# Kernel optimization log

Hardware: AMD Instinct MI355X
Metric: run time of the kernel (lower is better)

Reference implementation:

```python
import jax, jax.numpy as jnp
import numpy as np

L = 16384   # sequence length
H = 1024    # feature dim
P = 1024    # state dim (ssm_size=2048, conj_sym=True -> P = ssm_size//2)
STEP_RESCALE = 1.0
CLIP_MAX = -1e-4


def setup_inputs() -> dict:
    key = jax.random.key(0)
    ks = jax.random.split(key, 7)
    log_dt_min, log_dt_max = np.log(0.001), np.log(0.1)
    return {
        "input_sequence": jax.random.normal(ks[0], (L, H), jnp.float32),
        # stable eigenvalues: negative real part
        "Lambda_re": -(jnp.abs(jax.random.normal(ks[1], (P,), jnp.float32)) + 1e-3),
        "Lambda_im": jax.random.normal(ks[2], (P,), jnp.float32) * jnp.pi,
        "B": jax.random.normal(ks[3], (P, H, 2), jnp.float32) / np.sqrt(H),
        "C": jax.random.normal(ks[4], (H, P, 2), jnp.float32) / np.sqrt(P),
        "D": jax.random.normal(ks[5], (H,), jnp.float32),
        "log_step": jax.random.uniform(ks[6], (P, 1), jnp.float32,
                                        minval=log_dt_min, maxval=log_dt_max),
    }


def _binop(q_i, q_j):
    # binary operator of the linear recurrence (diagonal A)
    A_i, b_i = q_i
    A_j, b_j = q_j
    return (A_j * A_i, A_j * b_i + b_j)


def reference(input_sequence, Lambda_re, Lambda_im, B, C, D, log_step):
    # clip_eigs=True: clamp real part at -1e-4
    Lambda = jnp.minimum(Lambda_re, CLIP_MAX) + 1j * Lambda_im        # (P,) complex64
    B_tilde = B[..., 0] + 1j * B[..., 1]                              # (P, H)
    C_tilde = C[..., 0] + 1j * C[..., 1]                              # (H, P)
    step = STEP_RESCALE * jnp.exp(log_step[:, 0])                     # (P,)
    # ZOH discretisation
    Lambda_bar = jnp.exp(Lambda * step)                               # (P,)
    B_bar = ((Lambda_bar - 1.0) / Lambda)[:, None] * B_tilde          # (P, H)
    # input projection: (L,H) @ (H,P) -> (L,P) complex
    Bu = input_sequence.astype(B_bar.dtype) @ B_bar.T
    Lam = jnp.broadcast_to(Lambda_bar, Bu.shape)                      # (L, P)
    # parallel (Blelchley-style) associative scan over time
    _, xs = jax.lax.associative_scan(_binop, (Lam, Bu))               # (L, P)
    # output projection; conj_sym=True -> factor 2 on the real part
    ys = 2.0 * jnp.real(xs @ C_tilde.T)                               # (L, H)
    return ys + input_sequence * D
```

## Files before the change

kernel.cpp:

```cpp
#include <hip/hip_runtime.h>
#include <hip/hip_bf16.h>
#include <stdint.h>


#define L_SEQ 16384
#define H_DIM 1024
#define P_DIM 1024
#define NCH   256
#define TCH   64

typedef __bf16 bf16x8 __attribute__((ext_vector_type(8)));
typedef float  floatx4 __attribute__((ext_vector_type(4)));
using bf16 = __hip_bfloat16;

__device__ __forceinline__ void gld_lds16(const void* g, void* l) {
    __builtin_amdgcn_global_load_lds(
        (const __attribute__((address_space(1))) uint32_t*)g,
        (__attribute__((address_space(3))) uint32_t*)l, 16, 0, 0);
}

__device__ __forceinline__ float lo_bf(uint32_t v) { return __uint_as_float(v << 16); }
__device__ __forceinline__ float hi_bf(uint32_t v) { return __uint_as_float(v & 0xffff0000u); }
__device__ __forceinline__ uint32_t pack_bf(float r, float i) {
    bf16 rb = __float2bfloat16(r), ib = __float2bfloat16(i);
    return ((uint32_t)(*(uint16_t*)&ib) << 16) | (uint32_t)(*(uint16_t*)&rb);
}

__device__ __forceinline__ float rd(const void* p, size_t i, int f) {
    return f ? ((const float*)p)[i]
             : __bfloat162float(((const bf16*)p)[i]);
}

__device__ __forceinline__ int detect_f32(const uint16_t* u) {
    __shared__ int cnt;
    if (threadIdx.x == 0) cnt = 0;
    __syncthreads();
    int c = 0;
    #pragma unroll
    for (int i = 0; i < 8; ++i) {
        int e = (u[threadIdx.x * 8 + i] >> 7) & 0xFF;
        c += (e >= 134);
    }
    if (c) atomicAdd(&cnt, c);
    __syncthreads();
    return cnt > 32;
}

__global__ void convert_u(const void* __restrict__ uin, bf16* __restrict__ ub) {
    const int f = detect_f32((const uint16_t*)uin);
    const size_t g = (size_t)blockIdx.x * 256 + threadIdx.x;
    if (f) {
        const float4* s = (const float4*)uin + g * 2;
        float4 a = s[0], b = s[1];
        alignas(16) bf16 t[8] = {
            __float2bfloat16(a.x), __float2bfloat16(a.y),
            __float2bfloat16(a.z), __float2bfloat16(a.w),
            __float2bfloat16(b.x), __float2bfloat16(b.y),
            __float2bfloat16(b.z), __float2bfloat16(b.w)};
        ((uint4*)ub)[g] = *(const uint4*)t;
    } else {
        ((uint4*)ub)[g] = ((const uint4*)uin)[g];
    }
}

__global__ void prep_all(const void* __restrict__ u,
                         const void* __restrict__ Lre, const void* __restrict__ Lim,
                         const void* __restrict__ lstep, const void* __restrict__ B,
                         const void* __restrict__ C, const void* __restrict__ D,
                         bf16* __restrict__ W1t, bf16* __restrict__ W2t,
                         float* __restrict__ d_f,
                         float2* __restrict__ lam, float2* __restrict__ lamT) {
    const int f = detect_f32((const uint16_t*)u);
    const int p = blockIdx.x;
    float lr = fminf(rd(Lre, p, f), -1e-4f);
    float li = rd(Lim, p, f);
    float s  = expf(rd(lstep, p, f));
    float ea = expf(lr * s);
    float lbr = ea * cosf(li * s), lbi = ea * sinf(li * s);
    float dr = lbr - 1.0f, di = lbi;
    float den = lr * lr + li * li;
    float cr = (dr * lr + di * li) / den;
    float ci = (di * lr - dr * li) / den;
    if (threadIdx.x == 0) {
        lam[p] = make_float2(lbr, lbi);
        float tr = lbr, ti = lbi;
        #pragma unroll
        for (int q = 0; q < 6; ++q) {
            float nr = tr * tr - ti * ti, ni = 2.0f * tr * ti;
            tr = nr; ti = ni;
        }
        lamT[p] = make_float2(tr, ti);
        d_f[p] = rd(D, p, f);
    }
    for (int h = threadIdx.x; h < H_DIM; h += blockDim.x) {
        size_t base = ((size_t)p * H_DIM + h) * 2;
        float br = rd(B, base + 0, f);
        float bi = rd(B, base + 1, f);
        W1t[(size_t)(2 * p)     * H_DIM + h] = __float2bfloat16(cr * br - ci * bi);
        W1t[(size_t)(2 * p + 1) * H_DIM + h] = __float2bfloat16(cr * bi + ci * br);
    }
    const int h = blockIdx.x;
    for (int q = threadIdx.x; q < P_DIM; q += blockDim.x) {
        size_t base = ((size_t)h * P_DIM + q) * 2;
        W2t[(size_t)h * (2 * P_DIM) + 2 * q]     = __float2bfloat16( 2.0f * rd(C, base + 0, f));
        W2t[(size_t)h * (2 * P_DIM) + 2 * q + 1] = __float2bfloat16(-2.0f * rd(C, base + 1, f));
    }
}

template <int N, int K, int MODE>
__global__ __launch_bounds__(256) void gemm_bt(
    const bf16* __restrict__ A, const bf16* __restrict__ Bt,
    bf16* __restrict__ OutBF, float* __restrict__ OutF,
    const bf16* __restrict__ U, const float* __restrict__ Dvec,
    const float2* __restrict__ lam, float2* __restrict__ aggp) {
    constexpr int NXB = N / 128;
    __shared__ alignas(16) uint8_t smem[32768];
    uint8_t* sA = smem;
    uint8_t* sB = smem + 16384;

    const int tid  = threadIdx.x;
    const int wave = tid >> 6;
    const int lane = tid & 63;
    const int bid = blockIdx.x;
    const int xr  = bid & 7;
    const int jj  = bid >> 3;
    const int bx  = jj % NXB;
    const int by  = (jj / NXB) * 8 + xr;
    const int bm  = by * 128, bn = bx * 128;
    const int wm  = (wave >> 1) * 64, wn = (wave & 1) * 64;

    floatx4 acc[4][4] = {};

    const int fr   = lane & 15;
    const int kq   = lane >> 4;
    const int srow = tid >> 3;
    const int skc  = tid & 7;

    for (int k0 = 0; k0 < K; k0 += 64) {
        #pragma unroll
        for (int q = 0; q < 4; ++q) {
            const int row = q * 32 + srow;
            const int kcg = skc ^ (row & 7);
            gld_lds16(A  + (size_t)(bm + row) * K + k0 + kcg * 8,
                      sA + q * 4096 + wave * 1024);
            gld_lds16(Bt + (size_t)(bn + row) * K + k0 + kcg * 8,
                      sB + q * 4096 + wave * 1024);
        }
        __syncthreads();
        #pragma unroll
        for (int s = 0; s < 2; ++s) {
            bf16x8 af[4], bfr[4];
            #pragma unroll
            for (int mi = 0; mi < 4; ++mi) {
                const int row = wm + mi * 16 + fr;
                const int ch  = (s * 4 + kq) ^ (row & 7);
                af[mi] = *(const bf16x8*)(sA + row * 128 + ch * 16);
            }
            #pragma unroll
            for (int ni = 0; ni < 4; ++ni) {
                const int row = wn + ni * 16 + fr;
                const int ch  = (s * 4 + kq) ^ (row & 7);
                bfr[ni] = *(const bf16x8*)(sB + row * 128 + ch * 16);
            }
            #pragma unroll
            for (int mi = 0; mi < 4; ++mi)
                #pragma unroll
                for (int ni = 0; ni < 4; ++ni)
                    acc[mi][ni] = __builtin_amdgcn_mfma_f32_16x16x32_bf16(
                        af[mi], bfr[ni], acc[mi][ni], 0, 0, 0);
        }
        __syncthreads();
    }

    const int col0  = bn + wn + fr;
    const int rbase = bm + wm + kq * 4;
    #pragma unroll
    for (int mi = 0; mi < 4; ++mi) {
        #pragma unroll
        for (int rr = 0; rr < 4; ++rr) {
            const int row = rbase + mi * 16 + rr;
            #pragma unroll
            for (int ni = 0; ni < 4; ++ni) {
                const int c = col0 + ni * 16;
                float v = acc[mi][ni][rr];
                if (MODE == 2) {
                    float uu = __bfloat162float(U[(size_t)row * H_DIM + c]);
                    __builtin_nontemporal_store(v + uu * Dvec[c],
                                                &OutF[(size_t)row * N + c]);
                } else {
                    OutBF[(size_t)row * N + c] = __float2bfloat16(v);
                }
            }
        }
    }

    if (MODE == 1) {
        float2* wtab = (float2*)smem;
        {
            const int ql = tid >> 2;
            const int t0 = (tid & 3) * 16;
            float2 lb = lam[(bn >> 1) + ql];
            float tr = lb.x, ti = lb.y;
            #pragma unroll
            for (int q = 0; q < 4; ++q) {
                float nr = tr * tr - ti * ti, ni = 2.f * tr * ti;
                tr = nr; ti = ni;
            }
            float p32r = tr * tr - ti * ti, p32i = 2.f * tr * ti;
            float wr, wi;
            if (t0 == 0)       { wr = p32r * tr - p32i * ti; wi = p32r * ti + p32i * tr; }
            else if (t0 == 16) { wr = p32r; wi = p32i; }
            else if (t0 == 32) { wr = tr;   wi = ti; }
            else               { wr = 1.f;  wi = 0.f; }
            #pragma unroll
            for (int j = 15; j >= 0; --j) {
                wtab[ql * 64 + t0 + j] = make_float2(wr, wi);
                float nr = wr * lb.x - wi * lb.y;
                float ni = wr * lb.y + wi * lb.x;
                wr = nr; wi = ni;
            }
        }
        __syncthreads();
        const int par = fr & 1;
        const int cg  = (bm + wm) >> 6;
        #pragma unroll
        for (int ni = 0; ni < 4; ++ni) {
            const int ql = (wn + ni * 16 + (fr & ~1)) >> 1;
            float s = 0.f;
            #pragma unroll
            for (int mi = 0; mi < 4; ++mi)
                #pragma unroll
                for (int rr = 0; rr < 4; ++rr) {
                    const int t = mi * 16 + kq * 4 + rr;
                    float own  = acc[mi][ni][rr];
                    float part = __shfl_xor(own, 1);
                    float2 wv = wtab[ql * 64 + t];
                    s += wv.x * own + (par ? wv.y : -wv.y) * part;
                }
            s += __shfl_xor(s, 16);
            s += __shfl_xor(s, 32);
            float other = __shfl_xor(s, 1);
            if (kq == 0 && par == 0)
                aggp[(size_t)cg * P_DIM + (bn >> 1) + ql] = make_float2(s, other);
        }
    }
}

__global__ void scan_phase2p(const float2* __restrict__ agg,
                             const float2* __restrict__ lamT,
                             float2* __restrict__ carry) {
    const int w = threadIdx.x >> 6;
    const int j = threadIdx.x & 63;
    const int p = blockIdx.x * 4 + w;
    const float2 A = lamT[p];
    float b2r = A.x * A.x - A.y * A.y, b2i = 2.f * A.x * A.y;
    float Br = b2r * b2r - b2i * b2i, Bi = 2.f * b2r * b2i;
    float2 a[4];
    #pragma unroll
    for (int k = 0; k < 4; ++k) a[k] = agg[(size_t)(4 * j + k) * P_DIM + p];
    float xr = 0.f, xi = 0.f;
    #pragma unroll
    for (int k = 0; k < 4; ++k) {
        float nr = A.x * xr - A.y * xi + a[k].x;
        float ni = A.x * xi + A.y * xr + a[k].y;
        xr = nr; xi = ni;
    }
    float cr = Br, ci = Bi, vr = xr, vi = xi;
    #pragma unroll
    for (int d = 1; d < 64; d <<= 1) {
        float pvr = __shfl_up(vr, d), pvi = __shfl_up(vi, d);
        float pcr = __shfl_up(cr, d), pci = __shfl_up(ci, d);
        if (j >= d) {
            float nvr = cr * pvr - ci * pvi + vr;
            float nvi = cr * pvi + ci * pvr + vi;
            float ncr = cr * pcr - ci * pci;
            float nci = cr * pci + ci * pcr;
            vr = nvr; vi = nvi; cr = ncr; ci = nci;
        }
    }
    float sr = __shfl_up(vr, 1), si = __shfl_up(vi, 1);
    if (j == 0) { sr = 0.f; si = 0.f; }
    #pragma unroll
    for (int k = 0; k < 4; ++k) {
        carry[(size_t)(4 * j + k) * P_DIM + p] = make_float2(sr, si);
        float nr = A.x * sr - A.y * si + a[k].x;
        float ni = A.x * si + A.y * sr + a[k].y;
        sr = nr; si = ni;
    }
}

__global__ void scan_phase3(uint32_t* __restrict__ BuX,
                            const float2* __restrict__ lam,
                            const float2* __restrict__ carry) {
    const int p = blockIdx.y * 256 + threadIdx.x;
    const int c = blockIdx.x;
    const float2 lb = lam[p];
    const float2 c0 = carry[(size_t)c * P_DIM + p];
    float xr = c0.x, xi = c0.y;
    uint32_t* b = BuX + (size_t)c * TCH * P_DIM + p;
    #pragma unroll 4
    for (int j = 0; j < TCH; ++j) {
        uint32_t v = *b;
        float nr = lb.x * xr - lb.y * xi + lo_bf(v);
        float ni = lb.x * xi + lb.y * xr + hi_bf(v);
        xr = nr; xi = ni;
        *b = pack_bf(xr, xi);
        b += P_DIM;
    }
}

extern "C" void kernel_launch(void* const* d_in, const int* in_sizes, int n_in,
                              void* d_out, int out_size, void* d_ws, size_t ws_size,
                              hipStream_t stream) {
    float* out = (float*)d_out;

    char* w = (char*)d_ws;
    w += 256;
    float2* lam   = (float2*)w;  w += (size_t)P_DIM * 8;
    float2* lamT  = (float2*)w;  w += (size_t)P_DIM * 8;
    float*  d_f   = (float*)w;   w += (size_t)H_DIM * 4;
    float2* agg   = (float2*)w;  w += (size_t)NCH * P_DIM * 8;
    float2* carry = (float2*)w;  w += (size_t)NCH * P_DIM * 8;
    bf16*   W1t   = (bf16*)w;    w += (size_t)2 * P_DIM * H_DIM * 2;
    bf16*   W2t   = (bf16*)w;    w += (size_t)H_DIM * 2 * P_DIM * 2;
    bf16*   ub    = (bf16*)w;    w += (size_t)L_SEQ * H_DIM * 2;
    bf16*   Xbuf  = (bf16*)w;

    convert_u<<<(L_SEQ * H_DIM / 8) / 256, 256, 0, stream>>>(d_in[0], ub);
    prep_all<<<P_DIM, 256, 0, stream>>>(d_in[0], d_in[1], d_in[2], d_in[6],
                                        d_in[3], d_in[4], d_in[5],
                                        W1t, W2t, d_f, lam, lamT);

    gemm_bt<2 * P_DIM, H_DIM, 1><<<(2 * P_DIM / 128) * 128, 256, 0, stream>>>(
        ub, W1t, Xbuf, nullptr, nullptr, nullptr, lam, agg);

    scan_phase2p<<<P_DIM / 4, 256, 0, stream>>>(agg, lamT, carry);
    scan_phase3<<<dim3(NCH, P_DIM / 256), 256, 0, stream>>>(
        (uint32_t*)Xbuf, lam, carry);

    gemm_bt<H_DIM, 2 * P_DIM, 2><<<(H_DIM / 128) * 128, 256, 0, stream>>>(
        Xbuf, W2t, nullptr, out, ub, d_f, nullptr, nullptr);
}
```

Measured before the change: 361.9 us.

## Unfuse chunk-aggregate scan from first GEMM into separate scan_phase1 kernel

Moves the per-chunk scan aggregate computation out of the first GEMM epilogue (where it used an LDS power table, shuffles and a weighted reduction over accumulators) into a standalone scan_phase1 kernel. That kernel reads the bf16 Bu buffer back and runs a sequential 64-step recurrence per chunk and state. The GEMM template is split into two specialised kernels. This lightens the GEMM epilogue but adds a kernel launch and an extra full pass over the Bu buffer in memory. The aggregate is also now computed from bf16-rounded values rather than fp32 accumulators.

```diff
diff --git a/kernel.cpp b/kernel.cpp
--- a/kernel.cpp
+++ b/kernel.cpp
@@ -107,16 +107,13 @@
     }
 }
 
-template <int N, int K, int MODE>
-__global__ __launch_bounds__(256) void gemm_bt(
+__global__ __launch_bounds__(256) void g1_bu(
     const bf16* __restrict__ A, const bf16* __restrict__ Bt,
-    bf16* __restrict__ OutBF, float* __restrict__ OutF,
-    const bf16* __restrict__ U, const float* __restrict__ Dvec,
-    const float2* __restrict__ lam, float2* __restrict__ aggp) {
+    bf16* __restrict__ OutBF) {
+    constexpr int N = 2 * P_DIM, K = H_DIM;
     constexpr int NXB = N / 128;
-    __shared__ alignas(16) uint8_t smem[32768];
-    uint8_t* sA = smem;
-    uint8_t* sB = smem + 16384;
+    __shared__ alignas(16) uint8_t sA[128 * 128];
+    __shared__ alignas(16) uint8_t sB[128 * 128];
 
     const int tid  = threadIdx.x;
     const int wave = tid >> 6;
@@ -182,68 +179,110 @@
             #pragma unroll
             for (int ni = 0; ni < 4; ++ni) {
                 const int c = col0 + ni * 16;
-                float v = acc[mi][ni][rr];
-                if (MODE == 2) {
-                    float uu = __bfloat162float(U[(size_t)row * H_DIM + c]);
-                    __builtin_nontemporal_store(v + uu * Dvec[c],
-                                                &OutF[(size_t)row * N + c]);
-                } else {
-                    OutBF[(size_t)row * N + c] = __float2bfloat16(v);
-                }
-            }
-        }
-    }
-
-    if (MODE == 1) {
-        float2* wtab = (float2*)smem;
-        {
-            const int ql = tid >> 2;
-            const int t0 = (tid & 3) * 16;
-            float2 lb = lam[(bn >> 1) + ql];
-            float tr = lb.x, ti = lb.y;
-            #pragma unroll
-            for (int q = 0; q < 4; ++q) {
-                float nr = tr * tr - ti * ti, ni = 2.f * tr * ti;
-                tr = nr; ti = ni;
-            }
-            float p32r = tr * tr - ti * ti, p32i = 2.f * tr * ti;
-            float wr, wi;
-            if (t0 == 0)       { wr = p32r * tr - p32i * ti; wi = p32r * ti + p32i * tr; }
-            else if (t0 == 16) { wr = p32r; wi = p32i; }
-            else if (t0 == 32) { wr = tr;   wi = ti; }
-            else               { wr = 1.f;  wi = 0.f; }
-            #pragma unroll
-            for (int j = 15; j >= 0; --j) {
-                wtab[ql * 64 + t0 + j] = make_float2(wr, wi);
-                float nr = wr * lb.x - wi * lb.y;
-                float ni = wr * lb.y + wi * lb.x;
-                wr = nr; wi = ni;
-            }
+                OutBF[(size_t)row * N + c] = __float2bfloat16(acc[mi][ni][rr]);
+            }
+        }
+    }
+}
+
+__global__ __launch_bounds__(256) void g2_out(
+    const bf16* __restrict__ A, const bf16* __restrict__ Bt,
+    float* __restrict__ OutF,
+    const bf16* __restrict__ U, const float* __restrict__ Dvec) {
+    constexpr int N = H_DIM, K = 2 * P_DIM;
+    constexpr int NXB = N / 128;
+    __shared__ alignas(16) uint8_t sA[128 * 128];
+    __shared__ alignas(16) uint8_t sB[128 * 128];
+
+    const int tid  = threadIdx.x;
+    const int wave = tid >> 6;
+    const int lane = tid & 63;
+    const int bid = blockIdx.x;
+    const int xr  = bid & 7;
+    const int jj  = bid >> 3;
+    const int bx  = jj % NXB;
+    const int by  = (jj / NXB) * 8 + xr;
+    const int bm  = by * 128, bn = bx * 128;
+    const int wm  = (wave >> 1) * 64, wn = (wave & 1) * 64;
+
+    floatx4 acc[4][4] = {};
+
+    const int fr   = lane & 15;
+    const int kq   = lane >> 4;
+    const int srow = tid >> 3;
+    const int skc  = tid & 7;
+
+    for (int k0 = 0; k0 < K; k0 += 64) {
+        #pragma unroll
+        for (int q = 0; q < 4; ++q) {
+            const int row = q * 32 + srow;
+            const int kcg = skc ^ (row & 7);
+            gld_lds16(A  + (size_t)(bm + row) * K + k0 + kcg * 8,
+                      sA + q * 4096 + wave * 1024);
+            gld_lds16(Bt + (size_t)(bn + row) * K + k0 + kcg * 8,
+                      sB + q * 4096 + wave * 1024);
         }
         __syncthreads();
-        const int par = fr & 1;
-        const int cg  = (bm + wm) >> 6;
-        #pragma unroll
-        for (int ni = 0; ni < 4; ++ni) {
-            const int ql = (wn + ni * 16 + (fr & ~1)) >> 1;
-            float s = 0.f;
+        #pragma unroll
+        for (int s = 0; s < 2; ++s) {
+            bf16x8 af[4], bfr[4];
+            #pragma unroll
+            for (int mi = 0; mi < 4; ++mi) {
+                const int row = wm + mi * 16 + fr;
+                const int ch  = (s * 4 + kq) ^ (row & 7);
+                af[mi] = *(const bf16x8*)(sA + row * 128 + ch * 16);
+            }
+            #pragma unroll
+            for (int ni = 0; ni < 4; ++ni) {
+                const int row = wn + ni * 16 + fr;
+                const int ch  = (s * 4 + kq) ^ (row & 7);
+                bfr[ni] = *(const bf16x8*)(sB + row * 128 + ch * 16);
+            }
             #pragma unroll
             for (int mi = 0; mi < 4; ++mi)
                 #pragma unroll
-                for (int rr = 0; rr < 4; ++rr) {
-                    const int t = mi * 16 + kq * 4 + rr;
-                    float own  = acc[mi][ni][rr];
-                    float part = __shfl_xor(own, 1);
-                    float2 wv = wtab[ql * 64 + t];
-                    s += wv.x * own + (par ? wv.y : -wv.y) * part;
-                }
-            s += __shfl_xor(s, 16);
-            s += __shfl_xor(s, 32);
-            float other = __shfl_xor(s, 1);
-            if (kq == 0 && par == 0)
-                aggp[(size_t)cg * P_DIM + (bn >> 1) + ql] = make_float2(s, other);
-        }
-    }
+                for (int ni = 0; ni < 4; ++ni)
+                    acc[mi][ni] = __builtin_amdgcn_mfma_f32_16x16x32_bf16(
+                        af[mi], bfr[ni], acc[mi][ni], 0, 0, 0);
+        }
+        __syncthreads();
+    }
+
+    const int col0  = bn + wn + fr;
+    const int rbase = bm + wm + kq * 4;
+    #pragma unroll
+    for (int mi = 0; mi < 4; ++mi) {
+        #pragma unroll
+        for (int rr = 0; rr < 4; ++rr) {
+            const int row = rbase + mi * 16 + rr;
+            #pragma unroll
+            for (int ni = 0; ni < 4; ++ni) {
+                const int c = col0 + ni * 16;
+                float uu = __bfloat162float(U[(size_t)row * H_DIM + c]);
+                __builtin_nontemporal_store(acc[mi][ni][rr] + uu * Dvec[c],
+                                            &OutF[(size_t)row * N + c]);
+            }
+        }
+    }
+}
+
+__global__ void scan_phase1(const uint32_t* __restrict__ Bu,
+                            const float2* __restrict__ lam,
+                            float2* __restrict__ agg) {
+    const int p = blockIdx.y * 256 + threadIdx.x;
+    const int c = blockIdx.x;
+    const float2 lb = lam[p];
+    float xr = 0.f, xi = 0.f;
+    const uint32_t* b = Bu + (size_t)c * TCH * P_DIM + p;
+    #pragma unroll 4
+    for (int j = 0; j < TCH; ++j) {
+        uint32_t v = *b;
+        float nr = lb.x * xr - lb.y * xi + lo_bf(v);
+        float ni = lb.x * xi + lb.y * xr + hi_bf(v);
+        xr = nr; xi = ni;
+        b += P_DIM;
+    }
+    agg[(size_t)c * P_DIM + p] = make_float2(xr, xi);
 }
 
 __global__ void scan_phase2p(const float2* __restrict__ agg,
@@ -331,13 +370,13 @@
                                         d_in[3], d_in[4], d_in[5],
                                         W1t, W2t, d_f, lam, lamT);
 
-    gemm_bt<2 * P_DIM, H_DIM, 1><<<(2 * P_DIM / 128) * 128, 256, 0, stream>>>(
-        ub, W1t, Xbuf, nullptr, nullptr, nullptr, lam, agg);
-
+    g1_bu<<<(2 * P_DIM / 128) * 128, 256, 0, stream>>>(ub, W1t, Xbuf);
+
+    scan_phase1<<<dim3(NCH, P_DIM / 256), 256, 0, stream>>>(
+        (const uint32_t*)Xbuf, lam, agg);
     scan_phase2p<<<P_DIM / 4, 256, 0, stream>>>(agg, lamT, carry);
     scan_phase3<<<dim3(NCH, P_DIM / 256), 256, 0, stream>>>(
         (uint32_t*)Xbuf, lam, carry);
 
-    gemm_bt<H_DIM, 2 * P_DIM, 2><<<(H_DIM / 128) * 128, 256, 0, stream>>>(
-        Xbuf, W2t, nullptr, out, ub, d_f, nullptr, nullptr);
-}
+    g2_out<<<(H_DIM / 128) * 128, 256, 0, stream>>>(Xbuf, W2t, out, ub, d_f);
+}
```

After: 354.6 us. 1.02x faster.
